# Kernel optimization log

Hardware: AMD Instinct MI355X
Metric: run time of the kernel (lower is better)

## Reference

```python
import jax, jax.numpy as jnp
import numpy as np

EPS = 1e-5
L = 512
P1 = 64  # patch_num + 1
B = 512
H = 2048


def layernorm2d(x, g, b):
    # LayerNorm over the last two dims [P1, L]
    mu = jnp.mean(x, axis=(-2, -1), keepdims=True)
    var = jnp.mean(jnp.square(x - mu), axis=(-2, -1), keepdims=True)
    return (x - mu) * jax.lax.rsqrt(var + EPS) * g + b


def freq_filter(x, w):
    # rfft(x) * rfft(w) then irfft, all with ortho normalization
    X = jnp.fft.rfft(x, axis=-1, norm='ortho')          # [B, P1, L//2+1]
    W = jnp.fft.rfft(w, axis=-1, norm='ortho')          # [1, L//2+1]
    return jnp.fft.irfft(X * W, n=L, axis=-1, norm='ortho')


def setup_inputs() -> dict:
    key = jax.random.key(0)
    ks = jax.random.split(key, 4)
    x = jax.random.normal(ks[0], (B, P1, L), dtype=jnp.float32)
    w = 0.02 * jax.random.normal(ks[1], (1, L), dtype=jnp.float32)
    w1 = jax.random.normal(ks[2], (L, H), dtype=jnp.float32) * (1.0 / np.sqrt(L))
    b1 = jnp.zeros((H,), jnp.float32)
    w2 = jax.random.normal(ks[3], (H, L), dtype=jnp.float32) * (1.0 / np.sqrt(H))
    b2 = jnp.zeros((L,), jnp.float32)
    return {
        'x': x, 'w': w,
        'ln1_w': jnp.ones((P1, L), jnp.float32), 'ln1_b': jnp.zeros((P1, L), jnp.float32),
        'ln2_w': jnp.ones((P1, L), jnp.float32), 'ln2_b': jnp.zeros((P1, L), jnp.float32),
        'w1': w1, 'b1': b1, 'w2': w2, 'b2': b2,
    }


def reference(x, w, ln1_w, ln1_b, ln2_w, ln2_b, w1, b1, w2, b2):
    res = x
    h = layernorm2d(x, ln1_w, ln1_b)
    h = freq_filter(h, w)
    # dropout is identity in inference
    h = layernorm2d(h, ln2_w, ln2_b)
    # PositionwiseFeedForward: Linear -> ReLU -> (dropout) -> Linear
    h = jax.nn.relu(jnp.einsum('bpl,lh->bph', h, w1) + b1)
    h = jnp.einsum('bph,hl->bpl', h, w2) + b2
    return h + res
```

## Files before the change

kernel.cpp:

```cpp
#include <hip/hip_runtime.h>

typedef __bf16  bf16x8 __attribute__((ext_vector_type(8)));
typedef float   f32x4  __attribute__((ext_vector_type(4)));
typedef unsigned short u16;

__device__ __forceinline__ u16 f2bf(float f) {
  union { float f; unsigned u32; } c; c.f = f;
  unsigned r = c.u32 + 0x7fffu + ((c.u32 >> 16) & 1u);
  return (u16)(r >> 16);
}
__device__ __forceinline__ float bf2f(u16 u) {
  union { unsigned u32; float f; } c; c.u32 = (unsigned)u << 16; return c.f;
}

__device__ __forceinline__ void async16(const void* g, void* l) {
  __builtin_amdgcn_global_load_lds(
      (const __attribute__((address_space(1))) unsigned*)g,
      (__attribute__((address_space(3))) unsigned*)l, 16, 0, 0);
}

__global__ __launch_bounds__(256) void build_ct(const float* __restrict__ w,
                                                u16* __restrict__ ct) {
  int idx = blockIdx.x * 256 + threadIdx.x;
  int n = idx >> 9, k = idx & 511;
  float v = w[(n - k) & 511] * 0.04419417382415922f;
  ct[idx] = f2bf(v);
}

__global__ __launch_bounds__(256) void transpose_w(const float* __restrict__ in,
                                                   u16* __restrict__ out,
                                                   int R, int C) {
  __shared__ float tile[32][33];
  int bx = blockIdx.x * 32;
  int by = blockIdx.y * 32;
  int tx = threadIdx.x & 31, ty = threadIdx.x >> 5;
#pragma unroll
  for (int r = ty; r < 32; r += 8)
    tile[r][tx] = in[(size_t)(by + r) * C + bx + tx];
  __syncthreads();
#pragma unroll
  for (int r = ty; r < 32; r += 8)
    out[(size_t)(bx + r) * R + by + tx] = f2bf(tile[tx][r]);
}

__global__ __launch_bounds__(512, 2) void ln_f32(const float* __restrict__ x,
                                                 const float* __restrict__ g,
                                                 const float* __restrict__ beta,
                                                 u16* __restrict__ out) {
  const int tid = threadIdx.x;
  const size_t base = (size_t)blockIdx.x * 32768;
  float4 v[16];
  float s = 0.f, ss = 0.f;
#pragma unroll
  for (int j = 0; j < 16; ++j) {
    v[j] = *(const float4*)(x + base + tid * 4 + j * 2048);
    s  += v[j].x + v[j].y + v[j].z + v[j].w;
    ss += v[j].x * v[j].x + v[j].y * v[j].y + v[j].z * v[j].z + v[j].w * v[j].w;
  }
#pragma unroll
  for (int off = 32; off > 0; off >>= 1) {
    s += __shfl_down(s, off, 64);
    ss += __shfl_down(ss, off, 64);
  }
  __shared__ float red[16];
  int wave = tid >> 6, lane = tid & 63;
  if (lane == 0) { red[wave] = s; red[8 + wave] = ss; }
  __syncthreads();
  float S = 0.f, SS = 0.f;
#pragma unroll
  for (int wv = 0; wv < 8; ++wv) { S += red[wv]; SS += red[8 + wv]; }
  const float inv = 1.0f / 32768.0f;
  float mu = S * inv;
  float rs = rsqrtf(SS * inv - mu * mu + 1e-5f);
#pragma unroll
  for (int j = 0; j < 16; ++j) {
    const int i = tid * 4 + j * 2048;
    float4 gv = *(const float4*)(g + i);
    float4 bv = *(const float4*)(beta + i);
    uint2 o;
    o.x = (unsigned)f2bf((v[j].x - mu) * rs * gv.x + bv.x) |
          ((unsigned)f2bf((v[j].y - mu) * rs * gv.y + bv.y) << 16);
    o.y = (unsigned)f2bf((v[j].z - mu) * rs * gv.z + bv.z) |
          ((unsigned)f2bf((v[j].w - mu) * rs * gv.w + bv.w) << 16);
    *(uint2*)(out + base + i) = o;
  }
}

__global__ __launch_bounds__(512, 2) void ln_bf16(const u16* __restrict__ x,
                                                  const float* __restrict__ g,
                                                  const float* __restrict__ beta,
                                                  u16* __restrict__ out) {
  const int tid = threadIdx.x;
  const size_t base = (size_t)blockIdx.x * 32768;
  uint4 v[8];
  float s = 0.f, ss = 0.f;
#pragma unroll
  for (int j = 0; j < 8; ++j) {
    v[j] = *(const uint4*)(x + base + tid * 8 + j * 4096);
    const unsigned* a = &v[j].x;
#pragma unroll
    for (int t = 0; t < 4; ++t) {
      float lo = bf2f((u16)(a[t] & 0xffff)), hi = bf2f((u16)(a[t] >> 16));
      s += lo + hi; ss += lo * lo + hi * hi;
    }
  }
#pragma unroll
  for (int off = 32; off > 0; off >>= 1) {
    s += __shfl_down(s, off, 64);
    ss += __shfl_down(ss, off, 64);
  }
  __shared__ float red[16];
  int wave = tid >> 6, lane = tid & 63;
  if (lane == 0) { red[wave] = s; red[8 + wave] = ss; }
  __syncthreads();
  float S = 0.f, SS = 0.f;
#pragma unroll
  for (int wv = 0; wv < 8; ++wv) { S += red[wv]; SS += red[8 + wv]; }
  const float inv = 1.0f / 32768.0f;
  float mu = S * inv;
  float rs = rsqrtf(SS * inv - mu * mu + 1e-5f);
#pragma unroll
  for (int j = 0; j < 8; ++j) {
    const int i = tid * 8 + j * 4096;
    const unsigned* a = &v[j].x;
    uint4 o;
    unsigned* ov = &o.x;
#pragma unroll
    for (int t = 0; t < 4; ++t) {
      float lo = bf2f((u16)(a[t] & 0xffff)), hi = bf2f((u16)(a[t] >> 16));
      float4 gv2; float2 bv2;
      float glo = g[i + 2 * t], ghi = g[i + 2 * t + 1];
      float blo = beta[i + 2 * t], bhi = beta[i + 2 * t + 1];
      (void)gv2; (void)bv2;
      ov[t] = (unsigned)f2bf((lo - mu) * rs * glo + blo) |
              ((unsigned)f2bf((hi - mu) * rs * ghi + bhi) << 16);
    }
    *(uint4*)(out + base + i) = o;
  }
}

template <int MODE>
__global__ __launch_bounds__(256, 4) void gemm_bt(
    const u16* __restrict__ A, const u16* __restrict__ Bt,
    const float* __restrict__ bias, const float* __restrict__ resid,
    float* __restrict__ Cf, u16* __restrict__ Cb, int M, int N, int K) {
  __shared__ u16 As[128 * 64];
  __shared__ u16 Bs[128 * 64];
  const int tid = threadIdx.x;
  const int wave = tid >> 6, lane = tid & 63;
  const int quad = lane >> 4, l16 = lane & 15;
  const int wm = (wave >> 1) * 64, wn = (wave & 1) * 64;
  const int m0 = blockIdx.x * 128, n0 = blockIdx.y * 128;

  f32x4 acc[4][4];
#pragma unroll
  for (int i = 0; i < 4; ++i)
#pragma unroll
    for (int j = 0; j < 4; ++j) acc[i][j] = (f32x4){0.f, 0.f, 0.f, 0.f};

  const int rbase = tid >> 3;
  const int slot  = tid & 7;
  const int gcol  = (slot ^ (rbase & 7)) * 8;
  const int lofs  = tid * 8;

  const u16* ag = A + (size_t)(m0 + rbase) * K + gcol;
  const u16* bg = Bt + (size_t)(n0 + rbase) * K + gcol;
  const int swr = (l16 & 7);

  for (int k0 = 0; k0 < K; k0 += 64) {
    __syncthreads();
#pragma unroll
    for (int j = 0; j < 4; ++j) {
      async16(ag + (size_t)(32 * j) * K + k0, &As[lofs + j * 2048]);
      async16(bg + (size_t)(32 * j) * K + k0, &Bs[lofs + j * 2048]);
    }
    __syncthreads();
#pragma unroll
    for (int h = 0; h < 2; ++h) {
      const int sw = (((h << 2) + quad) ^ swr) * 8;
      bf16x8 af[4], bfr[4];
#pragma unroll
      for (int i = 0; i < 4; ++i)
        af[i] = *(const bf16x8*)&As[(wm + i * 16 + l16) * 64 + sw];
#pragma unroll
      for (int j = 0; j < 4; ++j)
        bfr[j] = *(const bf16x8*)&Bs[(wn + j * 16 + l16) * 64 + sw];
#pragma unroll
      for (int i = 0; i < 4; ++i)
#pragma unroll
        for (int j = 0; j < 4; ++j)
          acc[i][j] = __builtin_amdgcn_mfma_f32_16x16x32_bf16(af[i], bfr[j],
                                                              acc[i][j], 0, 0, 0);
    }
  }

#pragma unroll
  for (int j = 0; j < 4; ++j) {
    const int col = n0 + wn + j * 16 + l16;
    float bj = 0.f;
    if (MODE >= 1) bj = bias[col];
#pragma unroll
    for (int i = 0; i < 4; ++i) {
      const int rowb = m0 + wm + i * 16 + quad * 4;
#pragma unroll
      for (int r = 0; r < 4; ++r) {
        float v = acc[i][j][r] + bj;
        if (MODE == 1) v = fmaxf(v, 0.f);
        size_t idx = (size_t)(rowb + r) * N + col;
        if (MODE == 2) { v += resid[idx]; Cf[idx] = v; }
        else           Cb[idx] = f2bf(v);
      }
    }
  }
}

extern "C" void kernel_launch(void* const* d_in, const int* in_sizes, int n_in,
                              void* d_out, int out_size, void* d_ws,
                              size_t ws_size, hipStream_t stream) {
  const float* x    = (const float*)d_in[0];
  const float* w    = (const float*)d_in[1];
  const float* ln1w = (const float*)d_in[2];
  const float* ln1b = (const float*)d_in[3];
  const float* ln2w = (const float*)d_in[4];
  const float* ln2b = (const float*)d_in[5];
  const float* w1   = (const float*)d_in[6];
  const float* b1   = (const float*)d_in[7];
  const float* w2   = (const float*)d_in[8];
  const float* b2   = (const float*)d_in[9];
  float* out = (float*)d_out;

  char* ws = (char*)d_ws;
  u16*   y   = (u16*)(ws);
  u16*   h1  = (u16*)(ws);
  u16*   h2  = (u16*)(ws + 33554432);
  u16*   h3  = (u16*)(ws + 134217728);
  u16*   ct  = (u16*)(ws + 167772160);
  u16*   w1t = (u16*)(ws + 168296448);
  u16*   w2t = (u16*)(ws + 170393600);

  build_ct<<<1024, 256, 0, stream>>>(w, ct);
  transpose_w<<<dim3(64, 16), 256, 0, stream>>>(w1, w1t, 512, 2048);
  transpose_w<<<dim3(16, 64), 256, 0, stream>>>(w2, w2t, 2048, 512);

  ln_f32<<<512, 512, 0, stream>>>(x, ln1w, ln1b, h1);
  gemm_bt<0><<<dim3(256, 4), 256, 0, stream>>>(h1, ct, nullptr, nullptr,
                                               nullptr, h2, 32768, 512, 512);
  ln_bf16<<<512, 512, 0, stream>>>(h2, ln2w, ln2b, h3);
  gemm_bt<1><<<dim3(256, 16), 256, 0, stream>>>(h3, w1t, b1, nullptr,
                                                nullptr, y, 32768, 2048, 512);
  gemm_bt<2><<<dim3(256, 4), 256, 0, stream>>>(y, w2t, b2, x,
                                               out, nullptr, 32768, 512, 2048);
}
```

Baseline: 382.8 us.

## Rewrite GEMM with 256x256 tiles, 32x32 MFMA, multi-buffered async loads and XCD remap

```diff
diff --git a/kernel.cpp b/kernel.cpp
--- a/kernel.cpp
+++ b/kernel.cpp
@@ -1,7 +1,7 @@
 #include <hip/hip_runtime.h>
 
 typedef __bf16  bf16x8 __attribute__((ext_vector_type(8)));
-typedef float   f32x4  __attribute__((ext_vector_type(4)));
+typedef float   f32x16 __attribute__((ext_vector_type(16)));
 typedef unsigned short u16;
 
 __device__ __forceinline__ u16 f2bf(float f) {
@@ -128,10 +128,8 @@
 #pragma unroll
     for (int t = 0; t < 4; ++t) {
       float lo = bf2f((u16)(a[t] & 0xffff)), hi = bf2f((u16)(a[t] >> 16));
-      float4 gv2; float2 bv2;
       float glo = g[i + 2 * t], ghi = g[i + 2 * t + 1];
       float blo = beta[i + 2 * t], bhi = beta[i + 2 * t + 1];
-      (void)gv2; (void)bv2;
       ov[t] = (unsigned)f2bf((lo - mu) * rs * glo + blo) |
               ((unsigned)f2bf((hi - mu) * rs * ghi + bhi) << 16);
     }
@@ -140,76 +138,103 @@
 }
 
 template <int MODE>
-__global__ __launch_bounds__(256, 4) void gemm_bt(
+__global__ __launch_bounds__(512, 2) void gemm_bt(
     const u16* __restrict__ A, const u16* __restrict__ Bt,
     const float* __restrict__ bias, const float* __restrict__ resid,
-    float* __restrict__ Cf, u16* __restrict__ Cb, int M, int N, int K) {
-  __shared__ u16 As[128 * 64];
-  __shared__ u16 Bs[128 * 64];
-  const int tid = threadIdx.x;
-  const int wave = tid >> 6, lane = tid & 63;
-  const int quad = lane >> 4, l16 = lane & 15;
-  const int wm = (wave >> 1) * 64, wn = (wave & 1) * 64;
-  const int m0 = blockIdx.x * 128, n0 = blockIdx.y * 128;
-
-  f32x4 acc[4][4];
-#pragma unroll
-  for (int i = 0; i < 4; ++i)
-#pragma unroll
-    for (int j = 0; j < 4; ++j) acc[i][j] = (f32x4){0.f, 0.f, 0.f, 0.f};
-
-  const int rbase = tid >> 3;
-  const int slot  = tid & 7;
-  const int gcol  = (slot ^ (rbase & 7)) * 8;
-  const int lofs  = tid * 8;
-
-  const u16* ag = A + (size_t)(m0 + rbase) * K + gcol;
-  const u16* bg = Bt + (size_t)(n0 + rbase) * K + gcol;
-  const int swr = (l16 & 7);
-
-  for (int k0 = 0; k0 < K; k0 += 64) {
-    __syncthreads();
-#pragma unroll
-    for (int j = 0; j < 4; ++j) {
-      async16(ag + (size_t)(32 * j) * K + k0, &As[lofs + j * 2048]);
-      async16(bg + (size_t)(32 * j) * K + k0, &Bs[lofs + j * 2048]);
-    }
-    __syncthreads();
-#pragma unroll
-    for (int h = 0; h < 2; ++h) {
-      const int sw = (((h << 2) + quad) ^ swr) * 8;
-      bf16x8 af[4], bfr[4];
-#pragma unroll
-      for (int i = 0; i < 4; ++i)
-        af[i] = *(const bf16x8*)&As[(wm + i * 16 + l16) * 64 + sw];
-#pragma unroll
-      for (int j = 0; j < 4; ++j)
-        bfr[j] = *(const bf16x8*)&Bs[(wn + j * 16 + l16) * 64 + sw];
-#pragma unroll
-      for (int i = 0; i < 4; ++i)
-#pragma unroll
-        for (int j = 0; j < 4; ++j)
-          acc[i][j] = __builtin_amdgcn_mfma_f32_16x16x32_bf16(af[i], bfr[j],
-                                                              acc[i][j], 0, 0, 0);
-    }
-  }
-
-#pragma unroll
-  for (int j = 0; j < 4; ++j) {
-    const int col = n0 + wn + j * 16 + l16;
+    float* __restrict__ Cf, u16* __restrict__ Cb,
+    int M, int N, int K, int MT) {
+  __shared__ u16 As[16384];
+  __shared__ u16 Bs[16384];
+
+  const int tid  = threadIdx.x;
+  const int lane = tid & 63;
+  const int wave = tid >> 6;
+  const int l31  = lane & 31, hi = lane >> 5;
+  const int wr = wave >> 2, wc = wave & 3;
+
+  const int nwg = gridDim.x;
+  const int q = nwg >> 3, r8 = nwg & 7;
+  const int xcd = blockIdx.x & 7, loc = blockIdx.x >> 3;
+  const int wgid =
+      (xcd < r8 ? xcd * (q + 1) : r8 * (q + 1) + (xcd - r8) * q) + loc;
+  const int bm = wgid % MT, bn = wgid / MT;
+  const int m0 = bm * 256, n0 = bn * 256;
+  (void)M;
+
+  const u16* ag = A  + (size_t)(m0 + (tid >> 1)) * K + (tid & 1) * 8;
+  const u16* bg = Bt + (size_t)(n0 + (tid >> 1)) * K + (tid & 1) * 8;
+
+  const int aoff = (wr * 128 + l31) * 16 + hi * 8;
+  const int boff = (wc * 64  + l31) * 16 + hi * 8;
+
+  f32x16 acc[4][2];
+#pragma unroll
+  for (int m = 0; m < 4; ++m)
+#pragma unroll
+    for (int n = 0; n < 2; ++n)
+#pragma unroll
+      for (int i = 0; i < 16; ++i) acc[m][n][i] = 0.f;
+
+  const int NT = K >> 4;
+
+  async16(ag,      As + tid * 8);
+  async16(bg,      Bs + tid * 8);
+  async16(ag + 16, As + 4096 + tid * 8);
+  async16(bg + 16, Bs + 4096 + tid * 8);
+  asm volatile("s_waitcnt vmcnt(2)" ::: "memory");
+  __builtin_amdgcn_sched_barrier(0);
+  __builtin_amdgcn_s_barrier();
+
+  for (int u = 0; u < NT; ++u) {
+    const int bb = (u & 3) * 4096;
+    bf16x8 av[4], bv[2];
+#pragma unroll
+    for (int m = 0; m < 4; ++m)
+      av[m] = *(const bf16x8*)&As[bb + aoff + m * 512];
+#pragma unroll
+    for (int n = 0; n < 2; ++n)
+      bv[n] = *(const bf16x8*)&Bs[bb + boff + n * 512];
+    if (u + 2 < NT) {
+      const int sb = ((u + 2) & 3) * 4096 + tid * 8;
+      async16(ag + (size_t)(u + 2) * 16, As + sb);
+      async16(bg + (size_t)(u + 2) * 16, Bs + sb);
+    }
+    __builtin_amdgcn_s_barrier();
+    asm volatile("s_waitcnt lgkmcnt(0)" ::: "memory");
+    __builtin_amdgcn_sched_barrier(0);
+    __builtin_amdgcn_s_setprio(1);
+#pragma unroll
+    for (int m = 0; m < 4; ++m)
+#pragma unroll
+      for (int n = 0; n < 2; ++n)
+        acc[m][n] = __builtin_amdgcn_mfma_f32_32x32x16_bf16(av[m], bv[n],
+                                                            acc[m][n], 0, 0, 0);
+    __builtin_amdgcn_s_setprio(0);
+    __builtin_amdgcn_sched_barrier(0);
+    if (u + 2 < NT) asm volatile("s_waitcnt vmcnt(2)" ::: "memory");
+    else            asm volatile("s_waitcnt vmcnt(0)" ::: "memory");
+    __builtin_amdgcn_sched_barrier(0);
+    __builtin_amdgcn_s_barrier();
+  }
+
+#pragma unroll
+  for (int n = 0; n < 2; ++n) {
+    const int col = n0 + wc * 64 + n * 32 + l31;
     float bj = 0.f;
     if (MODE >= 1) bj = bias[col];
 #pragma unroll
-    for (int i = 0; i < 4; ++i) {
-      const int rowb = m0 + wm + i * 16 + quad * 4;
-#pragma unroll
-      for (int r = 0; r < 4; ++r) {
-        float v = acc[i][j][r] + bj;
-        if (MODE == 1) v = fmaxf(v, 0.f);
-        size_t idx = (size_t)(rowb + r) * N + col;
-        if (MODE == 2) { v += resid[idx]; Cf[idx] = v; }
-        else           Cb[idx] = f2bf(v);
-      }
+    for (int m = 0; m < 4; ++m) {
+      const int row0 = m0 + wr * 128 + m * 32 + hi * 4;
+#pragma unroll
+      for (int g = 0; g < 4; ++g)
+#pragma unroll
+        for (int t = 0; t < 4; ++t) {
+          float v = acc[m][n][g * 4 + t] + bj;
+          if (MODE == 1) v = fmaxf(v, 0.f);
+          const size_t idx = (size_t)(row0 + g * 8 + t) * N + col;
+          if (MODE == 2) { v += resid[idx]; Cf[idx] = v; }
+          else           Cb[idx] = f2bf(v);
+        }
     }
   }
 }
@@ -243,11 +268,11 @@
   transpose_w<<<dim3(16, 64), 256, 0, stream>>>(w2, w2t, 2048, 512);
 
   ln_f32<<<512, 512, 0, stream>>>(x, ln1w, ln1b, h1);
-  gemm_bt<0><<<dim3(256, 4), 256, 0, stream>>>(h1, ct, nullptr, nullptr,
-                                               nullptr, h2, 32768, 512, 512);
+  gemm_bt<0><<<256, 512, 0, stream>>>(h1, ct, nullptr, nullptr,
+                                      nullptr, h2, 32768, 512, 512, 128);
   ln_bf16<<<512, 512, 0, stream>>>(h2, ln2w, ln2b, h3);
-  gemm_bt<1><<<dim3(256, 16), 256, 0, stream>>>(h3, w1t, b1, nullptr,
-                                                nullptr, y, 32768, 2048, 512);
-  gemm_bt<2><<<dim3(256, 4), 256, 0, stream>>>(y, w2t, b2, x,
-                                               out, nullptr, 32768, 512, 2048);
-}
+  gemm_bt<1><<<1024, 512, 0, stream>>>(h3, w1t, b1, nullptr,
+                                       nullptr, y, 32768, 2048, 512, 128);
+  gemm_bt<2><<<256, 512, 0, stream>>>(y, w2t, b2, x,
+                                      out, nullptr, 32768, 512, 2048, 128);
+}
```

New measurement: 401.1 us. 4.8% more time.

## Stage GEMM epilogue through LDS for coalesced stores, remap tiles per XCD, fuse setup

Applied to the files above, without the earlier changes.

```diff
diff --git a/kernel.cpp b/kernel.cpp
--- a/kernel.cpp
+++ b/kernel.cpp
@@ -19,20 +19,27 @@
       (__attribute__((address_space(3))) unsigned*)l, 16, 0, 0);
 }
 
-__global__ __launch_bounds__(256) void build_ct(const float* __restrict__ w,
-                                                u16* __restrict__ ct) {
-  int idx = blockIdx.x * 256 + threadIdx.x;
-  int n = idx >> 9, k = idx & 511;
-  float v = w[(n - k) & 511] * 0.04419417382415922f;
-  ct[idx] = f2bf(v);
-}
-
-__global__ __launch_bounds__(256) void transpose_w(const float* __restrict__ in,
-                                                   u16* __restrict__ out,
-                                                   int R, int C) {
+__global__ __launch_bounds__(256) void setup_all(
+    const float* __restrict__ w,  u16* __restrict__ ct,
+    const float* __restrict__ w1, u16* __restrict__ w1t,
+    const float* __restrict__ w2, u16* __restrict__ w2t) {
   __shared__ float tile[32][33];
-  int bx = blockIdx.x * 32;
-  int by = blockIdx.y * 32;
+  const int b = blockIdx.x;
+  if (b < 1024) {
+    int idx = b * 256 + threadIdx.x;
+    int n = idx >> 9, k = idx & 511;
+    float v = w[(n - k) & 511] * 0.04419417382415922f;
+    ct[idx] = f2bf(v);
+    return;
+  }
+  const float* in;  u16* out;  int R, C, bx, by;
+  if (b < 2048) {
+    int l = b - 1024; in = w1; out = w1t; R = 512;  C = 2048;
+    bx = (l & 63) * 32; by = (l >> 6) * 32;
+  } else {
+    int l = b - 2048; in = w2; out = w2t; R = 2048; C = 512;
+    bx = (l & 15) * 32; by = (l >> 4) * 32;
+  }
   int tx = threadIdx.x & 31, ty = threadIdx.x >> 5;
 #pragma unroll
   for (int r = ty; r < 32; r += 8)
@@ -128,10 +135,8 @@
 #pragma unroll
     for (int t = 0; t < 4; ++t) {
       float lo = bf2f((u16)(a[t] & 0xffff)), hi = bf2f((u16)(a[t] >> 16));
-      float4 gv2; float2 bv2;
       float glo = g[i + 2 * t], ghi = g[i + 2 * t + 1];
       float blo = beta[i + 2 * t], bhi = beta[i + 2 * t + 1];
-      (void)gv2; (void)bv2;
       ov[t] = (unsigned)f2bf((lo - mu) * rs * glo + blo) |
               ((unsigned)f2bf((hi - mu) * rs * ghi + bhi) << 16);
     }
@@ -143,14 +148,22 @@
 __global__ __launch_bounds__(256, 4) void gemm_bt(
     const u16* __restrict__ A, const u16* __restrict__ Bt,
     const float* __restrict__ bias, const float* __restrict__ resid,
-    float* __restrict__ Cf, u16* __restrict__ Cb, int M, int N, int K) {
-  __shared__ u16 As[128 * 64];
-  __shared__ u16 Bs[128 * 64];
+    float* __restrict__ Cf, u16* __restrict__ Cb, int M, int N, int K,
+    int NT) {
+  __shared__ u16 As[128 * 64] __attribute__((aligned(16)));
+  __shared__ u16 Bs[128 * 64] __attribute__((aligned(16)));
   const int tid = threadIdx.x;
   const int wave = tid >> 6, lane = tid & 63;
   const int quad = lane >> 4, l16 = lane & 15;
   const int wm = (wave >> 1) * 64, wn = (wave & 1) * 64;
-  const int m0 = blockIdx.x * 128, n0 = blockIdx.y * 128;
+
+  const int nwg = gridDim.x;
+  const int q8 = nwg >> 3, r8 = nwg & 7;
+  const int xcd = blockIdx.x & 7, loc = blockIdx.x >> 3;
+  const int wgid =
+      (xcd < r8 ? xcd * (q8 + 1) : r8 * (q8 + 1) + (xcd - r8) * q8) + loc;
+  const int m0 = (wgid / NT) * 128, n0 = (wgid % NT) * 128;
+  (void)M;
 
   f32x4 acc[4][4];
 #pragma unroll
@@ -194,22 +207,65 @@
     }
   }
 
-#pragma unroll
-  for (int j = 0; j < 4; ++j) {
-    const int col = n0 + wn + j * 16 + l16;
-    float bj = 0.f;
-    if (MODE >= 1) bj = bias[col];
-#pragma unroll
-    for (int i = 0; i < 4; ++i) {
-      const int rowb = m0 + wm + i * 16 + quad * 4;
-#pragma unroll
-      for (int r = 0; r < 4; ++r) {
-        float v = acc[i][j][r] + bj;
-        if (MODE == 1) v = fmaxf(v, 0.f);
-        size_t idx = (size_t)(rowb + r) * N + col;
-        if (MODE == 2) { v += resid[idx]; Cf[idx] = v; }
-        else           Cb[idx] = f2bf(v);
+  __syncthreads();
+
+  if (MODE != 2) {
+#pragma unroll
+    for (int h = 0; h < 2; ++h) {
+      if ((wave >> 1) == h) {
+#pragma unroll
+        for (int j = 0; j < 4; ++j) {
+          float bj = 0.f;
+          if (MODE >= 1) bj = bias[n0 + wn + j * 16 + l16];
+#pragma unroll
+          for (int i = 0; i < 4; ++i)
+#pragma unroll
+            for (int r = 0; r < 4; ++r) {
+              float v = acc[i][j][r] + bj;
+              if (MODE == 1) v = fmaxf(v, 0.f);
+              As[(i * 16 + quad * 4 + r) * 128 + wn + j * 16 + l16] = f2bf(v);
+            }
+        }
       }
+      __syncthreads();
+      const int row = tid >> 2;
+#pragma unroll
+      for (int c = 0; c < 4; ++c) {
+        const int ch = c * 4 + (tid & 3);
+        uint4 vv = *(const uint4*)&As[row * 128 + ch * 8];
+        *(uint4*)&Cb[(size_t)(m0 + h * 64 + row) * N + n0 + ch * 8] = vv;
+      }
+      __syncthreads();
+    }
+  } else {
+    float* SF = (float*)As;
+#pragma unroll
+    for (int p = 0; p < 4; ++p) {
+      if ((wave >> 1) == (p >> 1)) {
+        const int i0 = (p & 1) * 2;
+#pragma unroll
+        for (int j = 0; j < 4; ++j) {
+          const float bj = bias[n0 + wn + j * 16 + l16];
+#pragma unroll
+          for (int i2 = 0; i2 < 2; ++i2)
+#pragma unroll
+            for (int r = 0; r < 4; ++r)
+              SF[(i2 * 16 + quad * 4 + r) * 128 + wn + j * 16 + l16] =
+                  acc[i0 + i2][j][r] + bj;
+        }
+      }
+      __syncthreads();
+      const int row = tid >> 3;
+#pragma unroll
+      for (int c = 0; c < 4; ++c) {
+        const int ch = c * 8 + (tid & 7);
+        const size_t idx = (size_t)(m0 + p * 32 + row) * N + n0 + ch * 4;
+        float4 sv = *(const float4*)&SF[row * 128 + ch * 4];
+        float4 rv = *(const float4*)&resid[idx];
+        sv.x += rv.x; sv.y += rv.y; sv.z += rv.z; sv.w += rv.w;
+        *(float4*)&Cf[idx] = sv;
+      }
+      __syncthreads();
     }
   }
 }
@@ -238,16 +294,14 @@
   u16*   w1t = (u16*)(ws + 168296448);
   u16*   w2t = (u16*)(ws + 170393600);
 
-  build_ct<<<1024, 256, 0, stream>>>(w, ct);
-  transpose_w<<<dim3(64, 16), 256, 0, stream>>>(w1, w1t, 512, 2048);
-  transpose_w<<<dim3(16, 64), 256, 0, stream>>>(w2, w2t, 2048, 512);
+  setup_all<<<3072, 256, 0, stream>>>(w, ct, w1, w1t, w2, w2t);
 
   ln_f32<<<512, 512, 0, stream>>>(x, ln1w, ln1b, h1);
-  gemm_bt<0><<<dim3(256, 4), 256, 0, stream>>>(h1, ct, nullptr, nullptr,
-                                               nullptr, h2, 32768, 512, 512);
+  gemm_bt<0><<<1024, 256, 0, stream>>>(h1, ct, nullptr, nullptr,
+                                       nullptr, h2, 32768, 512, 512, 4);
   ln_bf16<<<512, 512, 0, stream>>>(h2, ln2w, ln2b, h3);
-  gemm_bt<1><<<dim3(256, 16), 256, 0, stream>>>(h3, w1t, b1, nullptr,
-                                                nullptr, y, 32768, 2048, 512);
-  gemm_bt<2><<<dim3(256, 4), 256, 0, stream>>>(y, w2t, b2, x,
-                                               out, nullptr, 32768, 512, 2048);
-}
+  gemm_bt<1><<<4096, 256, 0, stream>>>(h3, w1t, b1, nullptr,
+                                       nullptr, y, 32768, 2048, 512, 16);
+  gemm_bt<2><<<1024, 256, 0, stream>>>(y, w2t, b2, x,
+                                       out, nullptr, 32768, 512, 2048, 4);
+}
```

Result: faster. 331.9 us (-13.3%).
